# Kernel tuning notes

Measured on AMD Instinct MI355X. Metric: run time of the kernel, lower is better.

## Reference

```python
import jax, jax.numpy as jnp
import numpy as np

LEVELS = 3  # num_basis = 1 + 1 + 2 + 4 = 8


def _haar_basis(x):
    """Closed-form vectorized Haar basis, x: [B, F] raw inputs.

    Replaces the original nested per-feature/per-level/per-bucket mask loops:
    at each level only one bucket k = floor(u*freq) is active, with value
    +2^(level/2) on the left half of the bucket and -2^(level/2) on the right
    half (x == 1.0 falls in the right half of the last bucket, matching the
    torch edge-case handling).
    """
    u = (jnp.tanh(x) + 1.0) / 2.0  # normalize to [0, 1]
    cols = [jnp.ones_like(u)[..., None]]  # scaling function phi
    for level in range(LEVELS):
        freq = 2 ** level
        k = jnp.clip(jnp.floor(u * freq), 0, freq - 1).astype(jnp.int32)  # bucket idx
        mid = (k.astype(u.dtype) + 0.5) / freq
        amp = jnp.asarray(2.0 ** (level / 2), u.dtype)
        sign = jnp.where(u < mid, amp, -amp)  # [B, F]
        cols.append(jax.nn.one_hot(k, freq, dtype=u.dtype) * sign[..., None])
    return jnp.concatenate(cols, axis=-1)  # [B, F, num_basis]


def setup_inputs() -> dict:
    key = jax.random.key(0)
    k1, k2, k3 = jax.random.split(key, 3)
    B, F, O, NB = 32768, 1024, 64, 8
    x = jax.random.normal(k1, (B, F), dtype=jnp.float32)
    coeffs = jax.random.normal(k2, (F, O, NB), dtype=jnp.float32) * 0.05
    base_weight = jax.random.normal(k3, (F, O), dtype=jnp.float32) * 0.05
    return {"x": x, "coeffs": coeffs, "base_weight": base_weight}


def reference(x, coeffs, base_weight):
    basis = _haar_basis(x)                         # [B, F, NB]
    wave_out = jnp.einsum('bin,ion->bo', basis, coeffs)  # [B, O]
    out = wave_out + x @ base_weight               # residual path
    kl = jnp.zeros((1,), dtype=x.dtype)            # non-variational: kl = 0
    return (out, kl)
```

## Files before the change

kernel.cpp:

```cpp
#include <hip/hip_runtime.h>
#include <math.h>


typedef __attribute__((ext_vector_type(8))) short short8;
typedef __attribute__((ext_vector_type(4))) float f32x4;

__device__ __forceinline__ unsigned int f2bf(float f) {
  unsigned int u = __float_as_uint(f);
  u += 0x7FFFu + ((u >> 16) & 1u);
  return u >> 16;
}

__device__ __forceinline__ void gen_basis(int j, unsigned int* d) {
  d[0] = (j < 4) ? 0x3F803F80u : 0xBF803F80u;
  unsigned int sq1 = (j & 2) ? 0xBFB5u : 0x3FB5u;
  d[1] = (j & 4) ? (sq1 << 16) : sq1;
  unsigned long long sd2 = (j & 1) ? 0xC000ull : 0x4000ull;
  unsigned long long d23 = sd2 << ((j & 6) << 3);
  d[2] = (unsigned int)d23;
  d[3] = (unsigned int)(d23 >> 32);
}

#define BARRIER() __asm__ volatile("s_waitcnt lgkmcnt(0)\n\ts_barrier" ::: "memory")

__device__ __forceinline__ void build_half(const float4& xq,
                                           uint4* __restrict__ dst, int h) {
  float xv[4] = {xq.x, xq.y, xq.z, xq.w};
  float t8v[4];
  unsigned int bad = 0;
#pragma unroll
  for (int ff = 0; ff < 4; ++ff) {
    float e = __expf(2.0f * xv[ff]);
    float r = __builtin_amdgcn_rcpf(e + 1.0f);
    float t8 = __builtin_fmaf(-8.0f, r, 8.0f);
    float rn = rintf(t8);
    if (fabsf(t8 - rn) < 3e-5f) bad |= 1u << ff;
    t8v[ff] = t8;
  }
  if (__builtin_expect(bad != 0, 0)) {
#pragma unroll
    for (int ff = 0; ff < 4; ++ff)
      if (bad & (1u << ff)) {
        float tf = (float)tanh((double)xv[ff]);
        t8v[ff] = ((tf + 1.0f) * 0.5f) * 8.0f;
      }
  }
  unsigned int dw[18];
#pragma unroll
  for (int p = 0; p < 2; ++p) {
    int je = (int)t8v[2 * p];     je = je > 7 ? 7 : je;
    int jo = (int)t8v[2 * p + 1]; jo = jo > 7 ? 7 : jo;
    gen_basis(je, &dw[9 * p]);
    dw[9 * p + 4] = f2bf(xv[2 * p]) | (f2bf(xv[2 * p + 1]) << 16);
    gen_basis(jo, &dw[9 * p + 5]);
  }
  const int db = h ? 2 : 0;
  const int gb = h ? 5 : 0;
#pragma unroll
  for (int k = 0; k < 4; ++k) {
    uint4 qv;
    qv.x = dw[db + 4 * k];     qv.y = dw[db + 4 * k + 1];
    qv.z = dw[db + 4 * k + 2]; qv.w = dw[db + 4 * k + 3];
    dst[(gb + k) * 256] = qv;
  }
  uint2 hv;
  if (h) { hv.x = dw[0];  hv.y = dw[1];  }
  else   { hv.x = dw[16]; hv.y = dw[17]; }
  ((uint2*)(dst + 4 * 256))[h] = hv;
}

__global__ __launch_bounds__(256) void build_w(const float* __restrict__ coeffs,
                                               const float* __restrict__ bw,
                                               uint4* __restrict__ Wsw) {
  const int l = threadIdx.x & 63;
  const int t = threadIdx.x >> 6;
  const int g = blockIdx.x;
  const int c = g / 9, j = g - c * 9;
  const int R = c * 4 + (l >> 4);
  const int o = t * 16 + (l & 15);
  unsigned int dwv[4];
#pragma unroll
  for (int jj = 0; jj < 8; ++jj) {
    int d = 8 * j + jj;
    int p = d / 18;
    int e = d - p * 18;
    int f, n;
    if (e < 8)       { f = 8 * R + 2 * p;     n = e; }
    else if (e == 8) { f = 8 * R + 2 * p;     n = 8; }
    else if (e == 9) { f = 8 * R + 2 * p + 1; n = 8; }
    else             { f = 8 * R + 2 * p + 1; n = e - 10; }
    float v = (n < 8) ? coeffs[(f * 64 + o) * 8 + n] : bw[f * 64 + o];
    unsigned int hh = f2bf(v);
    if (jj & 1) dwv[jj >> 1] |= hh << 16; else dwv[jj >> 1] = hh;
  }
  uint4 qq; qq.x = dwv[0]; qq.y = dwv[1]; qq.z = dwv[2]; qq.w = dwv[3];
  Wsw[(g * 4 + t) * 64 + l] = qq;
}

__global__ __launch_bounds__(512, 4) void wavelet_gemm(const float* __restrict__ x,
                                                       const uint4* __restrict__ Wsw,
                                                       float* __restrict__ out,
                                                       int out_size) {
  __shared__ uint4 Albuf[2 * 9 * 256];
  const int tid = threadIdx.x;
  const int l = tid & 63;
  const int w = tid >> 6;
  const int q = l >> 4;
  const int mm = l & 15;
  const int mh = w >> 2;
  const int nq = w & 3;
  const int r = w & 3;
  const int h = w >> 2;
  const int m = l;
  const long rowbase = (long)blockIdx.x * 64;

  const int wr_off  = r * 64 + m;
  const int rd_base = q * 64 + mh * 32 + mm;

  f32x4 acc0 = (f32x4){0.f, 0.f, 0.f, 0.f};
  f32x4 acc1 = (f32x4){0.f, 0.f, 0.f, 0.f};

  const float* xrow = x + (rowbase + m) * 1024 + r * 8 + h * 4;

  float4 xa = *(const float4*)(xrow);
  build_half(xa, Albuf + wr_off, h);
  xa = *(const float4*)(xrow + 32);
  BARRIER();

  for (int c = 0; c < 32; ++c) {
    uint4* cur = Albuf + (c & 1) * 2304;
    uint4* nxt = Albuf + ((c + 1) & 1) * 2304;
    uint4 Bv[9];
#pragma unroll
    for (int s = 0; s < 9; ++s)
      Bv[s] = Wsw[((c * 9 + s) * 4 + nq) * 64 + l];
    if (c + 1 < 32) {
      build_half(xa, nxt + wr_off, h);
      if (c + 2 < 32) xa = *(const float4*)(xrow + (c + 2) * 32);
    }
#pragma unroll
    for (int s = 0; s < 9; ++s) {
      const uint4* rb = cur + s * 256 + rd_base;
      short8 a0 = __builtin_bit_cast(short8, rb[0]);
      short8 a1 = __builtin_bit_cast(short8, rb[16]);
      short8 Bt = __builtin_bit_cast(short8, Bv[s]);
      acc0 = __builtin_amdgcn_mfma_f32_16x16x32_bf16(a0, Bt, acc0, 0, 0, 0);
      acc1 = __builtin_amdgcn_mfma_f32_16x16x32_bf16(a1, Bt, acc1, 0, 0, 0);
    }
    BARRIER();
  }

  float* og = out + (size_t)rowbase * 64;
  const int col  = nq * 16 + mm;
  const int row0 = mh * 32 + q * 4;
#pragma unroll
  for (int j = 0; j < 4; ++j) og[(row0 + j) * 64 + col] = acc0[j];
#pragma unroll
  for (int j = 0; j < 4; ++j) og[(row0 + 16 + j) * 64 + col] = acc1[j];
  if (blockIdx.x == 0 && tid == 0) out[out_size - 1] = 0.0f;
}

extern "C" void kernel_launch(void* const* d_in, const int* in_sizes, int n_in,
                              void* d_out, int out_size, void* d_ws, size_t ws_size,
                              hipStream_t stream) {
  const float* x      = (const float*)d_in[0];
  const float* coeffs = (const float*)d_in[1];
  const float* bw     = (const float*)d_in[2];
  uint4* Wsw = (uint4*)d_ws;
  float* out = (float*)d_out;

  build_w<<<288, 256, 0, stream>>>(coeffs, bw, Wsw);
  wavelet_gemm<<<512, 512, 0, stream>>>(x, (const uint4*)Wsw, out, out_size);
}
```

Measured before the change: 240.9 us.

## Switch to 32x32x16 MFMA with split-K across waves and LDS reduction

Replaces the 16x16x32 bf16 MFMA tiling with 32x32x16 MFMAs. Each wave now owns a 32-column half of the output and a strided subset of the 9 K-slices (split-K over 4 groups), with build_w re-laid out to match. Partial accumulators are reduced through shared memory at the end and written with vectorized stores. This aims to cut per-wave B loads and LDS A reads per FLOP, at the cost of an extra LDS reduction pass and an uneven K split (3 vs 2 slices per wave).

```diff
diff --git a/kernel.cpp b/kernel.cpp
--- a/kernel.cpp
+++ b/kernel.cpp
@@ -4,6 +4,7 @@
 
 typedef __attribute__((ext_vector_type(8))) short short8;
 typedef __attribute__((ext_vector_type(4))) float f32x4;
+typedef __attribute__((ext_vector_type(16))) float f32x16;
 
 __device__ __forceinline__ unsigned int f2bf(float f) {
   unsigned int u = __float_as_uint(f);
@@ -22,6 +23,7 @@
 }
 
 #define BARRIER() __asm__ volatile("s_waitcnt lgkmcnt(0)\n\ts_barrier" ::: "memory")
+#define KEEP4(v) __asm__ volatile("" : "+v"((v).x), "+v"((v).y), "+v"((v).z), "+v"((v).w))
 
 __device__ __forceinline__ void build_half(const float4& xq,
                                            uint4* __restrict__ dst, int h) {
@@ -76,8 +78,9 @@
   const int t = threadIdx.x >> 6;
   const int g = blockIdx.x;
   const int c = g / 9, j = g - c * 9;
-  const int R = c * 4 + (l >> 4);
-  const int o = t * 16 + (l & 15);
+  const int u = t >> 1, nq = t & 1;
+  const int R = c * 4 + 2 * u + (l >> 5);
+  const int o = nq * 32 + (l & 31);
   unsigned int dwv[4];
 #pragma unroll
   for (int jj = 0; jj < 8; ++jj) {
@@ -97,66 +100,103 @@
   Wsw[(g * 4 + t) * 64 + l] = qq;
 }
 
+#define MFMA32(A, B, C) __builtin_amdgcn_mfma_f32_32x32x16_bf16( \
+    __builtin_bit_cast(short8, (A)), __builtin_bit_cast(short8, (B)), (C), 0, 0, 0)
+
+template <int NS>
+__device__ __forceinline__ void run_main(const float* __restrict__ xrow,
+                                         const uint4* __restrict__ Bsw,
+                                         uint4* __restrict__ Albuf,
+                                         f32x16& acc0, f32x16& acc1,
+                                         int s0, int nq, int l, int wr_off, int h) {
+  const int hi = l >> 5;
+  const int l31 = l & 31;
+  float4 xa = *(const float4*)(xrow);
+  build_half(xa, Albuf + wr_off, h);
+  xa = *(const float4*)(xrow + 32);
+  BARRIER();
+
+  for (int c = 0; c < 32; ++c) {
+    uint4* cur = Albuf + (c & 1) * 2304;
+    uint4* nxt = Albuf + ((c + 1) & 1) * 2304;
+    uint4 Bv[NS][2];
+#pragma unroll
+    for (int i = 0; i < NS; ++i) {
+      const uint4* wp = Bsw + (size_t)(((c * 9 + s0 + 4 * i) * 4 + nq) * 64) + l;
+      Bv[i][0] = wp[0];
+      Bv[i][1] = wp[128];
+    }
+    if (c + 1 < 32) {
+      build_half(xa, nxt + wr_off, h);
+      if (c + 2 < 32) xa = *(const float4*)(xrow + (c + 2) * 32);
+    }
+#pragma unroll
+    for (int i = 0; i < NS; ++i) { KEEP4(Bv[i][0]); KEEP4(Bv[i][1]); }
+#pragma unroll
+    for (int i = 0; i < NS; ++i) {
+      const int s = s0 + 4 * i;
+      const uint4* rb = cur + s * 256 + hi * 64 + l31;
+      uint4 a00 = rb[0];
+      uint4 a01 = rb[32];
+      uint4 a10 = rb[128];
+      uint4 a11 = rb[160];
+      acc0 = MFMA32(a00, Bv[i][0], acc0);
+      acc0 = MFMA32(a10, Bv[i][1], acc0);
+      acc1 = MFMA32(a01, Bv[i][0], acc1);
+      acc1 = MFMA32(a11, Bv[i][1], acc1);
+    }
+    BARRIER();
+  }
+}
+
 __global__ __launch_bounds__(512, 4) void wavelet_gemm(const float* __restrict__ x,
-                                                       const uint4* __restrict__ Wsw,
+                                                       const uint4* __restrict__ Bsw,
                                                        float* __restrict__ out,
                                                        int out_size) {
   __shared__ uint4 Albuf[2 * 9 * 256];
   const int tid = threadIdx.x;
   const int l = tid & 63;
   const int w = tid >> 6;
-  const int q = l >> 4;
-  const int mm = l & 15;
-  const int mh = w >> 2;
-  const int nq = w & 3;
+  const int nq = w & 1;
+  const int ks = w >> 1;
   const int r = w & 3;
   const int h = w >> 2;
   const int m = l;
   const long rowbase = (long)blockIdx.x * 64;
-
-  const int wr_off  = r * 64 + m;
-  const int rd_base = q * 64 + mh * 32 + mm;
-
-  f32x4 acc0 = (f32x4){0.f, 0.f, 0.f, 0.f};
-  f32x4 acc1 = (f32x4){0.f, 0.f, 0.f, 0.f};
+  const int wr_off = r * 64 + m;
+
+  f32x16 acc0 = {};
+  f32x16 acc1 = {};
 
   const float* xrow = x + (rowbase + m) * 1024 + r * 8 + h * 4;
 
-  float4 xa = *(const float4*)(xrow);
-  build_half(xa, Albuf + wr_off, h);
-  xa = *(const float4*)(xrow + 32);
+  if (ks == 0) run_main<3>(xrow, Bsw, Albuf, acc0, acc1, 0, nq, l, wr_off, h);
+  else         run_main<2>(xrow, Bsw, Albuf, acc0, acc1, ks, nq, l, wr_off, h);
+
+  float* P = (float*)Albuf;
+  float* Pk = P + ks * 4096;
+  const int col   = nq * 32 + (l & 31);
+  const int rbase = 4 * (l >> 5);
+#pragma unroll
+  for (int rg = 0; rg < 16; ++rg) {
+    const int grow = (rg & 3) + 8 * (rg >> 2) + rbase;
+    Pk[grow * 64 + col]        = acc0[rg];
+    Pk[(grow + 32) * 64 + col] = acc1[rg];
+  }
   BARRIER();
 
-  for (int c = 0; c < 32; ++c) {
-    uint4* cur = Albuf + (c & 1) * 2304;
-    uint4* nxt = Albuf + ((c + 1) & 1) * 2304;
-    uint4 Bv[9];
-#pragma unroll
-    for (int s = 0; s < 9; ++s)
-      Bv[s] = Wsw[((c * 9 + s) * 4 + nq) * 64 + l];
-    if (c + 1 < 32) {
-      build_half(xa, nxt + wr_off, h);
-      if (c + 2 < 32) xa = *(const float4*)(xrow + (c + 2) * 32);
-    }
-#pragma unroll
-    for (int s = 0; s < 9; ++s) {
-      const uint4* rb = cur + s * 256 + rd_base;
-      short8 a0 = __builtin_bit_cast(short8, rb[0]);
-      short8 a1 = __builtin_bit_cast(short8, rb[16]);
-      short8 Bt = __builtin_bit_cast(short8, Bv[s]);
-      acc0 = __builtin_amdgcn_mfma_f32_16x16x32_bf16(a0, Bt, acc0, 0, 0, 0);
-      acc1 = __builtin_amdgcn_mfma_f32_16x16x32_bf16(a1, Bt, acc1, 0, 0, 0);
-    }
-    BARRIER();
-  }
-
   float* og = out + (size_t)rowbase * 64;
-  const int col  = nq * 16 + mm;
-  const int row0 = mh * 32 + q * 4;
-#pragma unroll
-  for (int j = 0; j < 4; ++j) og[(row0 + j) * 64 + col] = acc0[j];
-#pragma unroll
-  for (int j = 0; j < 4; ++j) og[(row0 + 16 + j) * 64 + col] = acc1[j];
+  const int row = tid >> 3;
+  const int cb  = (tid & 7) * 8;
+  f32x4 v0 = *(const f32x4*)(P + row * 64 + cb);
+  f32x4 v1 = *(const f32x4*)(P + row * 64 + cb + 4);
+#pragma unroll
+  for (int k = 1; k < 4; ++k) {
+    v0 = v0 + *(const f32x4*)(P + k * 4096 + row * 64 + cb);
+    v1 = v1 + *(const f32x4*)(P + k * 4096 + row * 64 + cb + 4);
+  }
+  *(f32x4*)(og + row * 64 + cb)     = v0;
+  *(f32x4*)(og + row * 64 + cb + 4) = v1;
   if (blockIdx.x == 0 && tid == 0) out[out_size - 1] = 0.0f;
 }
 
```

After: 225.3 us. -6.5%, faster.
